# Kernel tuning notes

Hardware: AMD Instinct MI355X
Metric: run time of the kernel (lower is better)

The kernel has to match this reference:

```python
import jax, jax.numpy as jnp
import numpy as np

KS = 2
K = 3 * KS**2 + 3 * KS + 1  # 19 hex-stencil sites
MUL = 16                     # multiplicity of each irrep block
C0 = 0.28209479177387814     # Y_0 integral-normalized, 1/(2*sqrt(pi))
C1 = 0.4886025119029199      # Y_1 coeff, sqrt(3/(4*pi))


def _hex_offsets(ks):
    """Hexagonal stencil offsets in the exact order of spin2coltri2d (center first)."""
    hexagon = [[1, 1], [1, 0], [0, -1], [-1, -1], [-1, 0], [0, 1]]
    offs = [(0, 0)]
    for k in range(1, ks + 1):
        for l in range(6 * k):
            eb = hexagon[l // k]
            ea = hexagon[(l // k + 1) % 6]
            offs.append((eb[0] * (k - l % k) + ea[0] * (l % k),
                         eb[1] * (k - l % k) + ea[1] * (l % k)))
    return offs  # length K


def setup_inputs() -> dict:
    key = jax.random.key(0)
    k1, k2, k3, k4, k5, k6, k7 = jax.random.split(key, 7)
    N, Lx, Ly = 4, 128, 128
    feat = jax.random.normal(k1, (N, Lx, Ly, 4 * MUL), dtype=jnp.float32)
    spin = jax.random.normal(k2, (N, Lx, Ly, 3), dtype=jnp.float32)
    # 'uvw' TensorProduct weights: one (mul_in, mul_out) block per hex position per path
    wshape = (K, MUL, MUL)
    w000 = jax.random.normal(k3, wshape, dtype=jnp.float32)  # 0e x 0e -> 0e
    w011 = jax.random.normal(k4, wshape, dtype=jnp.float32)  # 0e x 1e -> 1e
    w101 = jax.random.normal(k5, wshape, dtype=jnp.float32)  # 1e x 0e -> 1e
    w110 = jax.random.normal(k6, wshape, dtype=jnp.float32)  # 1e x 1e -> 0e (dot)
    w111 = jax.random.normal(k7, wshape, dtype=jnp.float32)  # 1e x 1e -> 1e (cross)
    return {"feat": feat, "spin": spin, "w000": w000, "w011": w011,
            "w101": w101, "w110": w110, "w111": w111}


def reference(feat, spin, w000, w011, w101, w110, w111):
    # --- spin2coltri2d: circular hex-stencil gather via rolls (no pad copy) ---
    offs = _hex_offsets(KS)
    col = jnp.stack([jnp.roll(feat, shift=(-ox, -oy), axis=(1, 2))
                     for (ox, oy) in offs], axis=3)  # (N,Lx,Ly,K,64)
    s = col[..., :MUL]                                       # scalars (N,Lx,Ly,K,16)
    v = col[..., MUL:].reshape(col.shape[:4] + (MUL, 3))     # vectors (N,Lx,Ly,K,16,3)
    # --- spherical harmonics of spin, l=0..1, normalize=False, integral norm ---
    sh1 = C1 * spin[..., jnp.array([1, 2, 0])]               # e3nn l=1 order (y,z,x)
    # --- CG tensor product, path-normalized per output irrep ---
    a_s = 1.0 / np.sqrt(2 * K * MUL)   # two paths feed scalar out
    a_v = 1.0 / np.sqrt(3 * K * MUL)   # three paths feed vector out
    out_s = C0 * jnp.einsum('nxyku,kuw->nxyw', s, w000)
    out_s = out_s + jnp.einsum('nxykui,nxyi,kuw->nxyw', v, sh1, w110) / np.sqrt(3.0)
    out_s = a_s * out_s
    out_v = jnp.einsum('nxyku,nxyi,kuw->nxywi', s, sh1, w011)
    out_v = out_v + C0 * jnp.einsum('nxykui,kuw->nxywi', v, w101)
    cross = jnp.cross(v, sh1[:, :, :, None, None, :])        # 1e x 1e -> 1e
    out_v = out_v + jnp.einsum('nxykui,kuw->nxywi', cross, w111) / np.sqrt(2.0)
    out_v = a_v * out_v
    return jnp.concatenate(
        [out_s, out_v.reshape(out_v.shape[:3] + (3 * MUL,))], axis=-1)
```

## Files before the change

### kernel.cpp

```cpp
#include <hip/hip_runtime.h>

typedef __attribute__((ext_vector_type(8))) short short8;
typedef __attribute__((ext_vector_type(4))) float f32x4;
typedef __attribute__((ext_vector_type(4))) int i32x4;

#define C0F 0.28209479177387814f
#define C1F 0.4886025119029199f
#define IS3 0.5773502691896258f
#define IS2 0.7071067811865476f
#define ASC 0.040555354f
#define AVC 0.033113308f

#define WBYTES 51200
#define FLDS   51200
#define LDS_TOTAL (51200 + 18432)

__constant__ int c_doff[20] = {0, 13, 12, -1, -13, -12, 1,
                               26, 25, 24, 11, -2, -14, -26, -25, -24, -11, 2, 14, 0};

__device__ inline unsigned short f32_bf16(float x) {
    unsigned int u = __float_as_uint(x);
    return (unsigned short)((u + 0x7FFF + ((u >> 16) & 1)) >> 16);
}

#define GLD16(gp, lp) __builtin_amdgcn_global_load_lds( \
    (const __attribute__((address_space(1))) unsigned int*)(gp), \
    (__attribute__((address_space(3))) unsigned int*)(lp), 16, 0, 0)

__global__ __launch_bounds__(256) void prep_kernel(
    const float* __restrict__ feat,
    const float* __restrict__ w000, const float* __restrict__ w011,
    const float* __restrict__ w101, const float* __restrict__ w110,
    const float* __restrict__ w111, unsigned char* __restrict__ ws)
{
    const int t = threadIdx.x;
    if (blockIdx.x >= 2048) {
        int o = (blockIdx.x - 2048) * 256 + t;
        int m = o / 5120;
        int r1 = o - m * 5120;
        int tap = r1 >> 8;
        int r2 = r1 & 255;
        int w = r2 >> 4;
        int u = r2 & 15;
        const float* W = (m == 0) ? w000 : (m == 1) ? w011 : (m == 2) ? w101 : (m == 3) ? w110 : w111;
        float val = (tap < 19) ? W[tap * 256 + u * 16 + w] : 0.0f;
        ((unsigned short*)ws)[o] = f32_bf16(val);
        return;
    }
    __shared__ float raw[2048];
    const int P0 = blockIdx.x * 32;
    const float4* src = (const float4*)feat + (size_t)P0 * 16;
    float4 l0 = src[t * 2];
    float4 l1 = src[t * 2 + 1];
    *(float4*)&raw[t * 8] = l0;
    *(float4*)&raw[t * 8 + 4] = l1;
    __syncthreads();
    const int p = t >> 3;
    const int c = t & 7;
    const float* r = &raw[p * 64];
    int ch0, stride;
    if (c < 2) { ch0 = c * 8; stride = 1; }
    else { int i = (c - 2) >> 1, uh = (c - 2) & 1; ch0 = 16 + i + 24 * uh; stride = 3; }
    unsigned int pk[4];
#pragma unroll
    for (int e = 0; e < 4; ++e) {
        unsigned int lo = f32_bf16(r[ch0 + stride * (2 * e)]);
        unsigned int hi = f32_bf16(r[ch0 + stride * (2 * e + 1)]);
        pk[e] = lo | (hi << 16);
    }
    const int PX = P0 + p;
    const int gy = PX & 127, gx = (PX >> 7) & 127;
    const int k = (4 * gx + gy + 2) & 7;
    *(i32x4*)(ws + WBYTES + (size_t)PX * 128 + ((c ^ k) << 4)) = *(const i32x4*)pk;
}

__global__ __launch_bounds__(256) void spinconv_mfma(
    const unsigned char* __restrict__ ws, const float* __restrict__ spin,
    float* __restrict__ out)
{
    extern __shared__ char smem[];
    const int tid = threadIdx.x, b = blockIdx.x;
    const int n = b >> 8;
    const int X0 = ((b >> 4) & 15) << 3;
    const int Y0 = (b & 15) << 3;
    const int lane = tid & 63, wv = tid >> 6;
    const int lx = lane & 15;
    const int q = lane >> 4;

    float sp[12];
#pragma unroll
    for (int r = 0; r < 4; ++r) {
        const int pl = (wv << 4) + (q << 2) + r;
        const int P = ((((n << 7) + X0 + (pl >> 3)) << 7) + Y0 + (pl & 7));
        sp[r * 3 + 0] = spin[3 * P + 0];
        sp[r * 3 + 1] = spin[3 * P + 1];
        sp[r * 3 + 2] = spin[3 * P + 2];
    }

    for (int j = 0; j < 13; ++j) {
        const int cid = j * 4 + wv;
        if (cid < 50)
            GLD16(ws + cid * 1024 + lane * 16, smem + cid * 1024);
    }
    const unsigned char* fsrc = ws + WBYTES;
    for (int j = 0; j < 5; ++j) {
        const int cid = wv + 4 * j;
        if (cid < 18) {
            const int px = cid * 8 + (lane >> 3);
            const int cc = lane & 7;
            const int dx = px / 12, dy = px - dx * 12;
            const int gx = (X0 - 2 + dx) & 127;
            const int gy = (Y0 - 2 + dy) & 127;
            GLD16(fsrc + (size_t)((((n << 7) + gx) << 7) + gy) * 128 + cc * 16,
                  smem + FLDS + cid * 1024);
        }
    }
    __syncthreads();

    const int u0b = (q & 1) << 4;
    const int taph = q >> 1;
    const int ploc = (wv << 4) + lx;
    const int slot0 = ((ploc >> 3) + 2) * 12 + ((ploc & 7) + 2);
    const char* flds = smem + FLDS;

    f32x4 aS0{0,0,0,0}, aS1{0,0,0,0};
    f32x4 aB0{0,0,0,0}, aB1{0,0,0,0}, aB2{0,0,0,0};
    f32x4 aC0{0,0,0,0}, aC1{0,0,0,0}, aC2{0,0,0,0};
    f32x4 aD0{0,0,0,0}, aD1{0,0,0,0}, aD2{0,0,0,0};

#pragma unroll
    for (int t = 0; t < 10; ++t) {
        const int tap = 2 * t + taph;
        const int st = slot0 + c_doff[tap];
        const char* ab = flds + st * 128;
        const int key = (st & 7) << 4;
        short8 a_s  = *(const short8*)(ab + ((u0b      ) ^ key));
        short8 a_v0 = *(const short8*)(ab + ((u0b + 32) ^ key));
        short8 a_v1 = *(const short8*)(ab + ((u0b + 64) ^ key));
        short8 a_v2 = *(const short8*)(ab + ((u0b + 96) ^ key));
        const char* bb = smem + tap * 512 + lx * 32 + u0b;
        short8 b000 = *(const short8*)(bb);
        short8 b011 = *(const short8*)(bb + 1 * 10240);
        short8 b101 = *(const short8*)(bb + 2 * 10240);
        short8 b110 = *(const short8*)(bb + 3 * 10240);
        short8 b111 = *(const short8*)(bb + 4 * 10240);
        aS0 = __builtin_amdgcn_mfma_f32_16x16x32_bf16(a_s,  b000, aS0, 0, 0, 0);
        aS1 = __builtin_amdgcn_mfma_f32_16x16x32_bf16(a_s,  b011, aS1, 0, 0, 0);
        aB0 = __builtin_amdgcn_mfma_f32_16x16x32_bf16(a_v0, b101, aB0, 0, 0, 0);
        aC0 = __builtin_amdgcn_mfma_f32_16x16x32_bf16(a_v0, b110, aC0, 0, 0, 0);
        aD0 = __builtin_amdgcn_mfma_f32_16x16x32_bf16(a_v0, b111, aD0, 0, 0, 0);
        aB1 = __builtin_amdgcn_mfma_f32_16x16x32_bf16(a_v1, b101, aB1, 0, 0, 0);
        aC1 = __builtin_amdgcn_mfma_f32_16x16x32_bf16(a_v1, b110, aC1, 0, 0, 0);
        aD1 = __builtin_amdgcn_mfma_f32_16x16x32_bf16(a_v1, b111, aD1, 0, 0, 0);
        aB2 = __builtin_amdgcn_mfma_f32_16x16x32_bf16(a_v2, b101, aB2, 0, 0, 0);
        aC2 = __builtin_amdgcn_mfma_f32_16x16x32_bf16(a_v2, b110, aC2, 0, 0, 0);
        aD2 = __builtin_amdgcn_mfma_f32_16x16x32_bf16(a_v2, b111, aD2, 0, 0, 0);
    }

    const int w = lx;
#pragma unroll
    for (int r = 0; r < 4; ++r) {
        const int pl = (wv << 4) + (q << 2) + r;
        const int gx = X0 + (pl >> 3);
        const int gy = Y0 + (pl & 7);
        const int P = (((n << 7) + gx) << 7) + gy;
        const float s0 = C1F * sp[r * 3 + 1];
        const float s1 = C1F * sp[r * 3 + 2];
        const float s2 = C1F * sp[r * 3 + 0];
        float* o = out + (size_t)P * 64;
        o[w] = ASC * (C0F * aS0[r] + IS3 * (s0 * aC0[r] + s1 * aC1[r] + s2 * aC2[r]));
        o[16 + 3 * w + 0] = AVC * (s0 * aS1[r] + C0F * aB0[r] + IS2 * (s2 * aD1[r] - s1 * aD2[r]));
        o[16 + 3 * w + 1] = AVC * (s1 * aS1[r] + C0F * aB1[r] + IS2 * (s0 * aD2[r] - s2 * aD0[r]));
        o[16 + 3 * w + 2] = AVC * (s2 * aS1[r] + C0F * aB2[r] + IS2 * (s1 * aD0[r] - s0 * aD1[r]));
    }
}

extern "C" void kernel_launch(void* const* d_in, const int* in_sizes, int n_in,
                              void* d_out, int out_size, void* d_ws, size_t ws_size,
                              hipStream_t stream) {
    const float* feat = (const float*)d_in[0];
    const float* spin = (const float*)d_in[1];
    const float* w000 = (const float*)d_in[2];
    const float* w011 = (const float*)d_in[3];
    const float* w101 = (const float*)d_in[4];
    const float* w110 = (const float*)d_in[5];
    const float* w111 = (const float*)d_in[6];
    float* out = (float*)d_out;
    unsigned char* ws = (unsigned char*)d_ws;

    static bool attr_set = false;
    if (!attr_set) {
        (void)hipFuncSetAttribute((const void*)spinconv_mfma,
                                  hipFuncAttributeMaxDynamicSharedMemorySize, LDS_TOTAL);
        attr_set = true;
    }

    hipLaunchKernelGGL(prep_kernel, dim3(2148), dim3(256), 0, stream,
                       feat, w000, w011, w101, w110, w111, ws);
    hipLaunchKernelGGL(spinconv_mfma, dim3(1024), dim3(256), LDS_TOTAL, stream,
                       ws, spin, out);
}
```

Baseline: 92.46 us.

## Double per-block tile to 8x16 pixels, reusing weight fragments across two rows

Each block now handles an 8x16 pixel tile instead of 8x8, and each wave computes two rows, so every B-fragment (weight) LDS read feeds twice as many MFMAs. The halo tile grows to 12x20 and the stencil offsets are adjusted to the new row pitch. The grid is halved to 512 blocks, which amortizes the per-block 50KB weight load and halo overhead. In exchange it doubles the accumulator registers, which may reduce occupancy, and leaves fewer blocks to fill the CUs.

```diff
diff --git a/kernel.cpp b/kernel.cpp
--- a/kernel.cpp
+++ b/kernel.cpp
@@ -11,12 +11,12 @@
 #define ASC 0.040555354f
 #define AVC 0.033113308f
 
-#define WBYTES 51200
-#define FLDS   51200
-#define LDS_TOTAL (51200 + 18432)
-
-__constant__ int c_doff[20] = {0, 13, 12, -1, -13, -12, 1,
-                               26, 25, 24, 11, -2, -14, -26, -25, -24, -11, 2, 14, 0};
+#define WB 51200
+#define FB 30720
+#define LDS_TOTAL (WB + FB)
+
+__constant__ int c_doff[20] = {0, 21,20,-1,-21,-20,1,
+                               42,41,40,19,-2,-22,-42,-41,-40,-19,2,22, 0};
 
 __device__ inline unsigned short f32_bf16(float x) {
     unsigned int u = __float_as_uint(x);
@@ -71,7 +71,7 @@
     const int PX = P0 + p;
     const int gy = PX & 127, gx = (PX >> 7) & 127;
     const int k = (4 * gx + gy + 2) & 7;
-    *(i32x4*)(ws + WBYTES + (size_t)PX * 128 + ((c ^ k) << 4)) = *(const i32x4*)pk;
+    *(i32x4*)(ws + WB + (size_t)PX * 128 + ((c ^ k) << 4)) = *(const i32x4*)pk;
 }
 
 __global__ __launch_bounds__(256) void spinconv_mfma(
@@ -80,98 +80,133 @@
 {
     extern __shared__ char smem[];
     const int tid = threadIdx.x, b = blockIdx.x;
-    const int n = b >> 8;
-    const int X0 = ((b >> 4) & 15) << 3;
-    const int Y0 = (b & 15) << 3;
+    const int n = b >> 7;
+    const int X0 = ((b >> 3) & 15) << 3;
+    const int Y0 = (b & 7) << 4;
     const int lane = tid & 63, wv = tid >> 6;
     const int lx = lane & 15;
     const int q = lane >> 4;
 
-    float sp[12];
-#pragma unroll
-    for (int r = 0; r < 4; ++r) {
-        const int pl = (wv << 4) + (q << 2) + r;
-        const int P = ((((n << 7) + X0 + (pl >> 3)) << 7) + Y0 + (pl & 7));
-        sp[r * 3 + 0] = spin[3 * P + 0];
-        sp[r * 3 + 1] = spin[3 * P + 1];
-        sp[r * 3 + 2] = spin[3 * P + 2];
-    }
+    float sp[24];
+#pragma unroll
+    for (int ti = 0; ti < 2; ++ti)
+#pragma unroll
+        for (int r = 0; r < 4; ++r) {
+            const int x = X0 + 2 * wv + ti;
+            const int y = Y0 + (q << 2) + r;
+            const int P = (((n << 7) + x) << 7) + y;
+            sp[ti * 12 + r * 3 + 0] = spin[3 * P + 0];
+            sp[ti * 12 + r * 3 + 1] = spin[3 * P + 1];
+            sp[ti * 12 + r * 3 + 2] = spin[3 * P + 2];
+        }
 
     for (int j = 0; j < 13; ++j) {
         const int cid = j * 4 + wv;
         if (cid < 50)
             GLD16(ws + cid * 1024 + lane * 16, smem + cid * 1024);
     }
-    const unsigned char* fsrc = ws + WBYTES;
-    for (int j = 0; j < 5; ++j) {
-        const int cid = wv + 4 * j;
-        if (cid < 18) {
-            const int px = cid * 8 + (lane >> 3);
+    const unsigned char* fsrc = ws + WB;
+    for (int j = 0; j < 8; ++j) {
+        const int cid = j * 4 + wv;
+        if (cid < 30) {
+            const int sl = cid * 8 + (lane >> 3);
             const int cc = lane & 7;
-            const int dx = px / 12, dy = px - dx * 12;
+            const int dx = sl / 20, dy = sl - dx * 20;
             const int gx = (X0 - 2 + dx) & 127;
             const int gy = (Y0 - 2 + dy) & 127;
             GLD16(fsrc + (size_t)((((n << 7) + gx) << 7) + gy) * 128 + cc * 16,
-                  smem + FLDS + cid * 1024);
+                  smem + WB + cid * 1024);
         }
     }
     __syncthreads();
 
     const int u0b = (q & 1) << 4;
     const int taph = q >> 1;
-    const int ploc = (wv << 4) + lx;
-    const int slot0 = ((ploc >> 3) + 2) * 12 + ((ploc & 7) + 2);
-    const char* flds = smem + FLDS;
-
-    f32x4 aS0{0,0,0,0}, aS1{0,0,0,0};
-    f32x4 aB0{0,0,0,0}, aB1{0,0,0,0}, aB2{0,0,0,0};
-    f32x4 aC0{0,0,0,0}, aC1{0,0,0,0}, aC2{0,0,0,0};
-    f32x4 aD0{0,0,0,0}, aD1{0,0,0,0}, aD2{0,0,0,0};
+    const char* flds = smem + WB;
+    const int s0a = (2 * wv + 2) * 20 + lx + 2;
+    const int s0b = s0a + 20;
+
+    f32x4 aS0{0,0,0,0}, aS1{0,0,0,0}, aB0{0,0,0,0}, aB1{0,0,0,0}, aB2{0,0,0,0},
+          aC0{0,0,0,0}, aC1{0,0,0,0}, aC2{0,0,0,0}, aD0{0,0,0,0}, aD1{0,0,0,0}, aD2{0,0,0,0};
+    f32x4 bS0{0,0,0,0}, bS1{0,0,0,0}, bB0{0,0,0,0}, bB1{0,0,0,0}, bB2{0,0,0,0},
+          bC0{0,0,0,0}, bC1{0,0,0,0}, bC2{0,0,0,0}, bD0{0,0,0,0}, bD1{0,0,0,0}, bD2{0,0,0,0};
 
 #pragma unroll
     for (int t = 0; t < 10; ++t) {
         const int tap = 2 * t + taph;
-        const int st = slot0 + c_doff[tap];
-        const char* ab = flds + st * 128;
-        const int key = (st & 7) << 4;
-        short8 a_s  = *(const short8*)(ab + ((u0b      ) ^ key));
-        short8 a_v0 = *(const short8*)(ab + ((u0b + 32) ^ key));
-        short8 a_v1 = *(const short8*)(ab + ((u0b + 64) ^ key));
-        short8 a_v2 = *(const short8*)(ab + ((u0b + 96) ^ key));
+        const int d = c_doff[tap];
+        const int stA = s0a + d;
+        const char* pa = flds + stA * 128;
+        const int ka = (stA & 7) << 4;
+        short8 xs  = *(const short8*)(pa + ((u0b      ) ^ ka));
+        short8 x0  = *(const short8*)(pa + ((u0b + 32) ^ ka));
+        short8 x1  = *(const short8*)(pa + ((u0b + 64) ^ ka));
+        short8 x2  = *(const short8*)(pa + ((u0b + 96) ^ ka));
+        const int stB = s0b + d;
+        const char* pb = flds + stB * 128;
+        const int kb = (stB & 7) << 4;
+        short8 ys  = *(const short8*)(pb + ((u0b      ) ^ kb));
+        short8 y0  = *(const short8*)(pb + ((u0b + 32) ^ kb));
+        short8 y1  = *(const short8*)(pb + ((u0b + 64) ^ kb));
+        short8 y2  = *(const short8*)(pb + ((u0b + 96) ^ kb));
         const char* bb = smem + tap * 512 + lx * 32 + u0b;
         short8 b000 = *(const short8*)(bb);
-        short8 b011 = *(const short8*)(bb + 1 * 10240);
-        short8 b101 = *(const short8*)(bb + 2 * 10240);
-        short8 b110 = *(const short8*)(bb + 3 * 10240);
-        short8 b111 = *(const short8*)(bb + 4 * 10240);
-        aS0 = __builtin_amdgcn_mfma_f32_16x16x32_bf16(a_s,  b000, aS0, 0, 0, 0);
-        aS1 = __builtin_amdgcn_mfma_f32_16x16x32_bf16(a_s,  b011, aS1, 0, 0, 0);
-        aB0 = __builtin_amdgcn_mfma_f32_16x16x32_bf16(a_v0, b101, aB0, 0, 0, 0);
-        aC0 = __builtin_amdgcn_mfma_f32_16x16x32_bf16(a_v0, b110, aC0, 0, 0, 0);
-        aD0 = __builtin_amdgcn_mfma_f32_16x16x32_bf16(a_v0, b111, aD0, 0, 0, 0);
-        aB1 = __builtin_amdgcn_mfma_f32_16x16x32_bf16(a_v1, b101, aB1, 0, 0, 0);
-        aC1 = __builtin_amdgcn_mfma_f32_16x16x32_bf16(a_v1, b110, aC1, 0, 0, 0);
-        aD1 = __builtin_amdgcn_mfma_f32_16x16x32_bf16(a_v1, b111, aD1, 0, 0, 0);
-        aB2 = __builtin_amdgcn_mfma_f32_16x16x32_bf16(a_v2, b101, aB2, 0, 0, 0);
-        aC2 = __builtin_amdgcn_mfma_f32_16x16x32_bf16(a_v2, b110, aC2, 0, 0, 0);
-        aD2 = __builtin_amdgcn_mfma_f32_16x16x32_bf16(a_v2, b111, aD2, 0, 0, 0);
+        short8 b011 = *(const short8*)(bb + 10240);
+        short8 b101 = *(const short8*)(bb + 20480);
+        short8 b110 = *(const short8*)(bb + 30720);
+        short8 b111 = *(const short8*)(bb + 40960);
+        aS0 = __builtin_amdgcn_mfma_f32_16x16x32_bf16(xs, b000, aS0, 0, 0, 0);
+        aS1 = __builtin_amdgcn_mfma_f32_16x16x32_bf16(xs, b011, aS1, 0, 0, 0);
+        aB0 = __builtin_amdgcn_mfma_f32_16x16x32_bf16(x0, b101, aB0, 0, 0, 0);
+        aC0 = __builtin_amdgcn_mfma_f32_16x16x32_bf16(x0, b110, aC0, 0, 0, 0);
+        aD0 = __builtin_amdgcn_mfma_f32_16x16x32_bf16(x0, b111, aD0, 0, 0, 0);
+        aB1 = __builtin_amdgcn_mfma_f32_16x16x32_bf16(x1, b101, aB1, 0, 0, 0);
+        aC1 = __builtin_amdgcn_mfma_f32_16x16x32_bf16(x1, b110, aC1, 0, 0, 0);
+        aD1 = __builtin_amdgcn_mfma_f32_16x16x32_bf16(x1, b111, aD1, 0, 0, 0);
+        aB2 = __builtin_amdgcn_mfma_f32_16x16x32_bf16(x2, b101, aB2, 0, 0, 0);
+        aC2 = __builtin_amdgcn_mfma_f32_16x16x32_bf16(x2, b110, aC2, 0, 0, 0);
+        aD2 = __builtin_amdgcn_mfma_f32_16x16x32_bf16(x2, b111, aD2, 0, 0, 0);
+        bS0 = __builtin_amdgcn_mfma_f32_16x16x32_bf16(ys, b000, bS0, 0, 0, 0);
+        bS1 = __builtin_amdgcn_mfma_f32_16x16x32_bf16(ys, b011, bS1, 0, 0, 0);
+        bB0 = __builtin_amdgcn_mfma_f32_16x16x32_bf16(y0, b101, bB0, 0, 0, 0);
+        bC0 = __builtin_amdgcn_mfma_f32_16x16x32_bf16(y0, b110, bC0, 0, 0, 0);
+        bD0 = __builtin_amdgcn_mfma_f32_16x16x32_bf16(y0, b111, bD0, 0, 0, 0);
+        bB1 = __builtin_amdgcn_mfma_f32_16x16x32_bf16(y1, b101, bB1, 0, 0, 0);
+        bC1 = __builtin_amdgcn_mfma_f32_16x16x32_bf16(y1, b110, bC1, 0, 0, 0);
+        bD1 = __builtin_amdgcn_mfma_f32_16x16x32_bf16(y1, b111, bD1, 0, 0, 0);
+        bB2 = __builtin_amdgcn_mfma_f32_16x16x32_bf16(y2, b101, bB2, 0, 0, 0);
+        bC2 = __builtin_amdgcn_mfma_f32_16x16x32_bf16(y2, b110, bC2, 0, 0, 0);
+        bD2 = __builtin_amdgcn_mfma_f32_16x16x32_bf16(y2, b111, bD2, 0, 0, 0);
     }
 
     const int w = lx;
 #pragma unroll
     for (int r = 0; r < 4; ++r) {
-        const int pl = (wv << 4) + (q << 2) + r;
-        const int gx = X0 + (pl >> 3);
-        const int gy = Y0 + (pl & 7);
-        const int P = (((n << 7) + gx) << 7) + gy;
-        const float s0 = C1F * sp[r * 3 + 1];
-        const float s1 = C1F * sp[r * 3 + 2];
-        const float s2 = C1F * sp[r * 3 + 0];
-        float* o = out + (size_t)P * 64;
-        o[w] = ASC * (C0F * aS0[r] + IS3 * (s0 * aC0[r] + s1 * aC1[r] + s2 * aC2[r]));
-        o[16 + 3 * w + 0] = AVC * (s0 * aS1[r] + C0F * aB0[r] + IS2 * (s2 * aD1[r] - s1 * aD2[r]));
-        o[16 + 3 * w + 1] = AVC * (s1 * aS1[r] + C0F * aB1[r] + IS2 * (s0 * aD2[r] - s2 * aD0[r]));
-        o[16 + 3 * w + 2] = AVC * (s2 * aS1[r] + C0F * aB2[r] + IS2 * (s1 * aD0[r] - s0 * aD1[r]));
+        const int y = Y0 + (q << 2) + r;
+        {
+            const int x = X0 + 2 * wv;
+            const int P = (((n << 7) + x) << 7) + y;
+            const float s0 = C1F * sp[r * 3 + 1];
+            const float s1 = C1F * sp[r * 3 + 2];
+            const float s2 = C1F * sp[r * 3 + 0];
+            float* o = out + (size_t)P * 64;
+            o[w] = ASC * (C0F * aS0[r] + IS3 * (s0 * aC0[r] + s1 * aC1[r] + s2 * aC2[r]));
+            o[16 + 3 * w + 0] = AVC * (s0 * aS1[r] + C0F * aB0[r] + IS2 * (s2 * aD1[r] - s1 * aD2[r]));
+            o[16 + 3 * w + 1] = AVC * (s1 * aS1[r] + C0F * aB1[r] + IS2 * (s0 * aD2[r] - s2 * aD0[r]));
+            o[16 + 3 * w + 2] = AVC * (s2 * aS1[r] + C0F * aB2[r] + IS2 * (s1 * aD0[r] - s0 * aD1[r]));
+        }
+        {
+            const int x = X0 + 2 * wv + 1;
+            const int P = (((n << 7) + x) << 7) + y;
+            const float s0 = C1F * sp[12 + r * 3 + 1];
+            const float s1 = C1F * sp[12 + r * 3 + 2];
+            const float s2 = C1F * sp[12 + r * 3 + 0];
+            float* o = out + (size_t)P * 64;
+            o[w] = ASC * (C0F * bS0[r] + IS3 * (s0 * bC0[r] + s1 * bC1[r] + s2 * bC2[r]));
+            o[16 + 3 * w + 0] = AVC * (s0 * bS1[r] + C0F * bB0[r] + IS2 * (s2 * bD1[r] - s1 * bD2[r]));
+            o[16 + 3 * w + 1] = AVC * (s1 * bS1[r] + C0F * bB1[r] + IS2 * (s0 * bD2[r] - s2 * bD0[r]));
+            o[16 + 3 * w + 2] = AVC * (s2 * bS1[r] + C0F * bB2[r] + IS2 * (s1 * bD0[r] - s0 * bD1[r]));
+        }
     }
 }
 
@@ -197,6 +232,6 @@
 
     hipLaunchKernelGGL(prep_kernel, dim3(2148), dim3(256), 0, stream,
                        feat, w000, w011, w101, w110, w111, ws);
-    hipLaunchKernelGGL(spinconv_mfma, dim3(1024), dim3(256), LDS_TOTAL, stream,
+    hipLaunchKernelGGL(spinconv_mfma, dim3(512), dim3(256), LDS_TOTAL, stream,
                        ws, spin, out);
 }
```

After: 90.22 us. 1.02x faster.
